# Kernel tuning notes

Hardware: AMD Instinct MI355X
Metric: run time of the kernel (lower is better)

The kernel has to match this reference:

```python
import jax, jax.numpy as jnp
import numpy as np

H, W = 16, 64
HK, WK = 7, 11
NUM_HEADS = 8
DIM = 512
HEAD_DIM = DIM // NUM_HEADS
SCALE = HEAD_DIM ** -0.5
N = H * W


def _local_mask():
    # Additive mask [N, N]: 0 inside the local window, -inf outside.
    # Equivalent to the torch loop: token (h,w) attends to (i,j) with
    # |i-h| <= HK//2 and |j-w| <= WK//2 (odd kernel, centered crop).
    h = jnp.arange(H)
    w = jnp.arange(W)
    hh, ww = jnp.meshgrid(h, w, indexing='ij')  # [H, W]
    q_h = hh.reshape(-1)  # [N]
    q_w = ww.reshape(-1)
    in_win = (jnp.abs(q_h[:, None] - q_h[None, :]) <= HK // 2) & \
             (jnp.abs(q_w[:, None] - q_w[None, :]) <= WK // 2)
    return jnp.where(in_win, 0.0, -jnp.inf).astype(jnp.float32)  # [N, N]


def setup_inputs() -> dict:
    key = jax.random.key(0)
    k1, k2, k3 = jax.random.split(key, 3)
    x = jax.random.normal(k1, (64, N, DIM), dtype=jnp.float32)
    w_qkv = jax.random.normal(k2, (DIM, 3 * DIM), dtype=jnp.float32) * 0.02
    w_proj = jax.random.normal(k3, (DIM, DIM), dtype=jnp.float32) * 0.02
    b_proj = jnp.zeros((DIM,), dtype=jnp.float32)
    return {"x": x, "w_qkv": w_qkv, "w_proj": w_proj, "b_proj": b_proj}


def reference(x, w_qkv, w_proj, b_proj):
    B = x.shape[0]
    mask = _local_mask()  # [N, N]
    qkv = (x @ w_qkv).reshape(B, N, 3, NUM_HEADS, HEAD_DIM)
    q = qkv[:, :, 0].transpose(0, 2, 1, 3) * SCALE  # [B, h, N, d]
    k = qkv[:, :, 1].transpose(0, 2, 1, 3)
    v = qkv[:, :, 2].transpose(0, 2, 1, 3)
    attn = jnp.einsum('bhnd,bhmd->bhnm', q, k) + mask  # [B, h, N, N]
    attn = jax.nn.softmax(attn, axis=-1)
    out = jnp.einsum('bhnm,bhmd->bhnd', attn, v)
    out = out.transpose(0, 2, 1, 3).reshape(B, N, DIM)
    return out @ w_proj + b_proj
```

## Files before the change

kernel.cpp:

```cpp
#include <hip/hip_runtime.h>
#include <hip/hip_bf16.h>
#include <stdint.h>

#define HGRID   16
#define WGRID   64
#define NTOK    1024
#define BATCH   64
#define NHEADS  8
#define HDIM    64
#define DMODEL  512
#define BH_TOT  512
#define QK_SCALE (0.125f * 1.44269504089f)

typedef __attribute__((ext_vector_type(8))) short short8;
typedef __attribute__((ext_vector_type(4))) float floatx4;

__device__ __forceinline__ short f2bf(float f) {
    union { float f; uint32_t u; } c{f};
    uint32_t r = (c.u + 0x7fffu + ((c.u >> 16) & 1u)) >> 16;
    return (short)r;
}

__device__ __forceinline__ void gload_lds16(const void* g, void* l) {
    auto gp = (const __attribute__((address_space(1))) void*)(uintptr_t)g;
    auto lp = (__attribute__((address_space(3))) void*)(uint32_t)(uintptr_t)l;
    __builtin_amdgcn_global_load_lds(gp, lp, 16, 0, 0);
}

__global__ __launch_bounds__(256)
void cast_x_kernel(const float* __restrict__ in, short* __restrict__ out) {
    size_t i = (size_t)blockIdx.x * 256 + threadIdx.x;
    const float4* in4 = (const float4*)in;
    float4 a = in4[i * 2];
    float4 b = in4[i * 2 + 1];
    short8 o;
    o[0] = f2bf(a.x); o[1] = f2bf(a.y); o[2] = f2bf(a.z); o[3] = f2bf(a.w);
    o[4] = f2bf(b.x); o[5] = f2bf(b.y); o[6] = f2bf(b.z); o[7] = f2bf(b.w);
    *(short8*)(out + i * 8) = o;
}

__global__ __launch_bounds__(256)
void tcast_kernel(const float* __restrict__ in, short* __restrict__ out, int R, int C) {
    __shared__ short tile[64][72];
    int r0 = blockIdx.x * 64, c0 = blockIdx.y * 64;
    int t = threadIdx.x;
#pragma unroll
    for (int i = 0; i < 16; i++) {
        int s = i * 256 + t;
        int r = s >> 6, c = s & 63;
        tile[r][c] = f2bf(in[(size_t)(r0 + r) * C + c0 + c]);
    }
    __syncthreads();
#pragma unroll
    for (int i = 0; i < 16; i++) {
        int s = i * 256 + t;
        int c = s >> 6, r = s & 63;
        out[(size_t)(c0 + c) * R + r0 + r] = tile[r][c];
    }
}

template <int MODE>
__global__ __launch_bounds__(256)
void gemm_kernel(const short* __restrict__ A, const short* __restrict__ Bm,
                 short* __restrict__ qo, short* __restrict__ ko, short* __restrict__ vo,
                 float* __restrict__ outf, const float* __restrict__ bias) {
    __shared__ short As[128 * 32];
    __shared__ short Bs[128 * 32];
    const int bn = blockIdx.x, bm = blockIdx.y;
    const int t = threadIdx.x;
    const int w = t >> 6;
    const int l = t & 63;
    const int wm = w >> 1, wn = w & 1;
    const int lq = l & 15, quad = l >> 4;

    const floatx4 zero = {0.f, 0.f, 0.f, 0.f};
    floatx4 acc[4][4];
#pragma unroll
    for (int i = 0; i < 4; i++)
#pragma unroll
        for (int j = 0; j < 4; j++) acc[i][j] = zero;

    const short* Ab = A + (size_t)bm * 128 * 512;
    const short* Bb = Bm + (size_t)bn * 128 * 512;

    for (int k0 = 0; k0 < 512; k0 += 32) {
        __syncthreads();
#pragma unroll
        for (int i = 0; i < 2; i++) {
            int s = i * 256 + t;
            int r = s >> 2, c8 = (s & 3) * 8;
            gload_lds16(Ab + (size_t)r * 512 + k0 + c8, &As[s * 8]);
            gload_lds16(Bb + (size_t)r * 512 + k0 + c8, &Bs[s * 8]);
        }
        __syncthreads();

        short8 af[4], bfr[4];
#pragma unroll
        for (int mi = 0; mi < 4; mi++)
            af[mi] = *(const short8*)&As[(wm * 64 + mi * 16 + lq) * 32 + quad * 8];
#pragma unroll
        for (int ni = 0; ni < 4; ni++)
            bfr[ni] = *(const short8*)&Bs[(wn * 64 + ni * 16 + lq) * 32 + quad * 8];
#pragma unroll
        for (int mi = 0; mi < 4; mi++)
#pragma unroll
            for (int ni = 0; ni < 4; ni++)
                acc[mi][ni] = __builtin_amdgcn_mfma_f32_16x16x32_bf16(
                    af[mi], bfr[ni], acc[mi][ni], 0, 0, 0);
    }

#pragma unroll
    for (int mi = 0; mi < 4; mi++)
#pragma unroll
        for (int ni = 0; ni < 4; ni++)
#pragma unroll
            for (int r = 0; r < 4; r++) {
                int row = bm * 128 + wm * 64 + mi * 16 + quad * 4 + r;
                int col = bn * 128 + wn * 64 + ni * 16 + lq;
                float val = acc[mi][ni][r];
                if (MODE == 0) {
                    int bidx = row >> 10, tok = row & 1023;
                    int which = col >> 9, hd = (col >> 6) & 7, dd = col & 63;
                    size_t didx = (((size_t)bidx * NHEADS + hd) * NTOK + tok) * HDIM + dd;
                    if (which == 0)       qo[didx] = f2bf(val * QK_SCALE);
                    else if (which == 1)  ko[didx] = f2bf(val);
                    else                  vo[didx] = f2bf(val);
                } else {
                    outf[(size_t)row * DMODEL + col] = val + bias[col];
                }
            }
}

__global__ __launch_bounds__(256)
void tv_kernel(const short* __restrict__ v, short* __restrict__ vT) {
    __shared__ short tile[64][72];
    int tt = blockIdx.x;
    int bh = blockIdx.y;
    int t = threadIdx.x;
    const short* src = v + ((size_t)bh * NTOK + tt * 64) * HDIM;
#pragma unroll
    for (int i = 0; i < 2; i++) {
        int s = i * 256 + t;
        int r = s >> 3, c8 = (s & 7) * 8;
        *(short8*)&tile[r][c8] = *(const short8*)(src + r * HDIM + c8);
    }
    __syncthreads();
    short* dst = vT + (size_t)bh * HDIM * NTOK + tt * 64;
#pragma unroll
    for (int i = 0; i < 2; i++) {
        int s = i * 256 + t;
        int d = s & 63, t0 = (s >> 6) * 8;
        short8 g;
#pragma unroll
        for (int j = 0; j < 8; j++) g[j] = tile[t0 + j][d];
        *(short8*)(dst + (size_t)d * NTOK + t0) = g;
    }
}

__global__ __launch_bounds__(256)
void attn_kernel(const short* __restrict__ q, const short* __restrict__ k,
                 const short* __restrict__ vT, short* __restrict__ ao) {
    const int bid = blockIdx.x;
    const int h = (bid >> 3) & 15;
    const int bh = (bid & 7) + 8 * (bid >> 7);
    const int b = bh >> 3, head = bh & 7;
    const int t = threadIdx.x;
    const int w = t >> 6;
    const int l = t & 63;
    const int lq = l & 15, quad = l >> 4;

    __shared__ short Kc[64][72];
    __shared__ short Vc[80][72];
    __shared__ short Pc[4][16][40];

    const int s_w = (w == 0) ? 0 : (w == 1) ? 8 : (w == 2) ? 24 : 32;

    const short* qbp = q + ((size_t)bh * NTOK + h * 64 + w * 16 + lq) * HDIM + quad * 8;
    short8 qa0 = *(const short8*)(qbp);
    short8 qa1 = *(const short8*)(qbp + 32);

    bool ok[2][4];
#pragma unroll
    for (int nt = 0; nt < 2; nt++)
#pragma unroll
        for (int r = 0; r < 4; r++) {
            int kw_g = s_w + nt * 16 + lq;
            int qi = w * 16 + quad * 4 + r;
            int dw = kw_g - qi;
            ok[nt][r] = (dw <= 5) && (dw >= -5);
        }

    const floatx4 zero = {0.f, 0.f, 0.f, 0.f};
    floatx4 O[5];
#pragma unroll
    for (int i = 0; i < 5; i++) O[i] = zero;

    if (t < 64) Vc[64][t] = (short)0x3F80;

    const int kh0 = (h - 3 < 0) ? 0 : h - 3;
    const int kh1 = (h + 3 > HGRID - 1) ? HGRID - 1 : h + 3;

    for (int kh = kh0; kh <= kh1; ++kh) {
        __syncthreads();
        {
            const short* kb = k + ((size_t)bh * NTOK + kh * 64) * HDIM;
            const short* vb = vT + (size_t)bh * HDIM * NTOK + kh * 64;
#pragma unroll
            for (int i = 0; i < 2; i++) {
                int s = i * 256 + t;
                int r = s >> 3, c8 = (s & 7) * 8;
                *(short8*)&Kc[r][c8] = *(const short8*)(kb + r * HDIM + c8);
                *(short8*)&Vc[r][c8] = *(const short8*)(vb + (size_t)r * NTOK + c8);
            }
        }
        __syncthreads();

        floatx4 S[2];
#pragma unroll
        for (int nt = 0; nt < 2; nt++) {
            S[nt] = zero;
            short8 b0 = *(const short8*)&Kc[s_w + nt * 16 + lq][quad * 8];
            short8 b1 = *(const short8*)&Kc[s_w + nt * 16 + lq][quad * 8 + 32];
            S[nt] = __builtin_amdgcn_mfma_f32_16x16x32_bf16(qa0, b0, S[nt], 0, 0, 0);
            S[nt] = __builtin_amdgcn_mfma_f32_16x16x32_bf16(qa1, b1, S[nt], 0, 0, 0);
        }

#pragma unroll
        for (int nt = 0; nt < 2; nt++)
#pragma unroll
            for (int r = 0; r < 4; r++) {
                float p = ok[nt][r] ? exp2f(S[nt][r]) : 0.f;
                Pc[w][quad * 4 + r][nt * 16 + lq] = f2bf(p);
            }

        short8 pa = *(const short8*)&Pc[w][lq][quad * 8];
#pragma unroll
        for (int dt = 0; dt < 5; dt++) {
            short8 vf = *(const short8*)&Vc[dt * 16 + lq][s_w + quad * 8];
            O[dt] = __builtin_amdgcn_mfma_f32_16x16x32_bf16(pa, vf, O[dt], 0, 0, 0);
        }
    }

    float inv[4];
#pragma unroll
    for (int r = 0; r < 4; r++) {
        float s = __shfl(O[4][r], l & 48);
        inv[r] = 1.0f / s;
    }

#pragma unroll
    for (int dt = 0; dt < 4; dt++)
#pragma unroll
        for (int r = 0; r < 4; r++) {
            int qi = w * 16 + quad * 4 + r;
            int d = dt * 16 + lq;
            float o = O[dt][r] * inv[r];
            ao[((size_t)b * NTOK + h * 64 + qi) * DMODEL + head * HDIM + d] = f2bf(o);
        }
}

extern "C" void kernel_launch(void* const* d_in, const int* in_sizes, int n_in,
                              void* d_out, int out_size, void* d_ws, size_t ws_size,
                              hipStream_t stream) {
    const float* x      = (const float*)d_in[0];
    const float* w_qkv  = (const float*)d_in[1];
    const float* w_proj = (const float*)d_in[2];
    const float* b_proj = (const float*)d_in[3];
    float* out = (float*)d_out;

    const size_t SZ_X    = (size_t)BATCH * NTOK * DMODEL * 2;
    const size_t SZ_HEAD = (size_t)BH_TOT * NTOK * HDIM * 2;
    char* p = (char*)d_ws;
    short* xb     = (short*)p; p += SZ_X;
    short* wqkvT  = (short*)p; p += (size_t)1536 * 512 * 2;
    short* wprojT = (short*)p; p += (size_t)512 * 512 * 2;
    short* qb     = (short*)p; p += SZ_HEAD;
    short* kb     = (short*)p; p += SZ_HEAD;
    short* vb     = (short*)p; p += SZ_HEAD;
    short* vTb    = (short*)p; p += SZ_HEAD;
    short* ao     = xb;

    cast_x_kernel<<<dim3((BATCH * NTOK * DMODEL) / (256 * 8)), dim3(256), 0, stream>>>(x, xb);
    tcast_kernel<<<dim3(512 / 64, 1536 / 64), dim3(256), 0, stream>>>(w_qkv, wqkvT, 512, 1536);
    tcast_kernel<<<dim3(512 / 64, 512 / 64), dim3(256), 0, stream>>>(w_proj, wprojT, 512, 512);
    gemm_kernel<0><<<dim3(1536 / 128, 65536 / 128), dim3(256), 0, stream>>>(
        xb, wqkvT, qb, kb, vb, nullptr, nullptr);
    tv_kernel<<<dim3(NTOK / 64, BH_TOT), dim3(256), 0, stream>>>(vb, vTb);
    attn_kernel<<<dim3(HGRID * BH_TOT), dim3(256), 0, stream>>>(qb, kb, vTb, ao);
    gemm_kernel<1><<<dim3(512 / 128, 65536 / 128), dim3(256), 0, stream>>>(
        ao, wprojT, nullptr, nullptr, nullptr, out, b_proj);
}
```

Measured before the change: 559.6 us.

## Replace GEMM with 256x256-tile, 8-wave, double-buffered swizzled LDS pipeline

Both projection GEMMs now use a new kernel with 512 threads and 256x256 output tiles. It keeps 128 KB of LDS in two buffers with an XOR swizzle, and issues direct global-to-LDS prefetches of the next K-slice interleaved with MFMA phases, using explicit barriers, waitcnt and setprio. It also remaps the block ID across groups of eight for better L2 locality. The aim is to raise MFMA utilisation and hide global load latency compared with the old single-buffered 128x128 kernel. In exchange it uses many registers and 128 KB of LDS per block, and its hand-tuned synchronisation is fragile.

```diff
diff --git a/kernel.cpp b/kernel.cpp
--- a/kernel.cpp
+++ b/kernel.cpp
@@ -25,6 +25,11 @@
     auto gp = (const __attribute__((address_space(1))) void*)(uintptr_t)g;
     auto lp = (__attribute__((address_space(3))) void*)(uint32_t)(uintptr_t)l;
     __builtin_amdgcn_global_load_lds(gp, lp, 16, 0, 0);
+}
+
+__device__ __forceinline__ void stage2(const short* g, char* l) {
+    gload_lds16(g, l);
+    gload_lds16(g + 32, l + 8192);
 }
 
 __global__ __launch_bounds__(256)
@@ -60,75 +65,198 @@
 }
 
 template <int MODE>
-__global__ __launch_bounds__(256)
-void gemm_kernel(const short* __restrict__ A, const short* __restrict__ Bm,
-                 short* __restrict__ qo, short* __restrict__ ko, short* __restrict__ vo,
-                 float* __restrict__ outf, const float* __restrict__ bias) {
-    __shared__ short As[128 * 32];
-    __shared__ short Bs[128 * 32];
-    const int bn = blockIdx.x, bm = blockIdx.y;
+__global__ __launch_bounds__(512, 2)
+void gemm8_kernel(const short* __restrict__ A, const short* __restrict__ Bm,
+                  short* __restrict__ qo, short* __restrict__ ko, short* __restrict__ vo,
+                  float* __restrict__ outf, const float* __restrict__ bias) {
+    constexpr int NBN = (MODE == 0) ? 6 : 2;
+    constexpr int NWG = (MODE == 0) ? 1536 : 512;
+    __shared__ short lds[65536];
+    char* ldsc = (char*)lds;
+
+    int bid = blockIdx.x;
+    bid = (bid & 7) * (NWG >> 3) + (bid >> 3);
+    const int bn = bid % NBN, bm = bid / NBN;
+
     const int t = threadIdx.x;
-    const int w = t >> 6;
-    const int l = t & 63;
-    const int wm = w >> 1, wn = w & 1;
+    const int w = t >> 6, l = t & 63;
     const int lq = l & 15, quad = l >> 4;
+    const int wm = w >> 2, wn = w & 3;
+
+    const int sw32 = ((lq >> 3) & 1) << 5;
+    const int qb16 = (quad * 16) ^ sw32;
+    const int a_lane = wm * 16384 + lq * 64 + qb16;
+    const int b_lane = 32768 + (wn >> 1) * 16384 + (wn & 1) * 4096 + lq * 64 + qb16;
+    const int t16 = t * 16;
+
+    const int srow = t >> 2;
+    const int scol = ((t & 3) * 8) ^ (((t >> 5) & 1) << 4);
+    const short* gA = A + (size_t)bm * 256 * 512 + (size_t)srow * 512 + scol;
+    const short* gB = Bm + (size_t)bn * 256 * 512 + (size_t)srow * 512 + scol;
 
     const floatx4 zero = {0.f, 0.f, 0.f, 0.f};
-    floatx4 acc[4][4];
-#pragma unroll
-    for (int i = 0; i < 4; i++)
+    floatx4 acc[8][4];
+#pragma unroll
+    for (int i = 0; i < 8; i++)
 #pragma unroll
         for (int j = 0; j < 4; j++) acc[i][j] = zero;
 
-    const short* Ab = A + (size_t)bm * 128 * 512;
-    const short* Bb = Bm + (size_t)bn * 128 * 512;
-
-    for (int k0 = 0; k0 < 512; k0 += 32) {
-        __syncthreads();
-#pragma unroll
-        for (int i = 0; i < 2; i++) {
-            int s = i * 256 + t;
-            int r = s >> 2, c8 = (s & 3) * 8;
-            gload_lds16(Ab + (size_t)r * 512 + k0 + c8, &As[s * 8]);
-            gload_lds16(Bb + (size_t)r * 512 + k0 + c8, &Bs[s * 8]);
-        }
-        __syncthreads();
-
-        short8 af[4], bfr[4];
-#pragma unroll
-        for (int mi = 0; mi < 4; mi++)
-            af[mi] = *(const short8*)&As[(wm * 64 + mi * 16 + lq) * 32 + quad * 8];
-#pragma unroll
-        for (int ni = 0; ni < 4; ni++)
-            bfr[ni] = *(const short8*)&Bs[(wn * 64 + ni * 16 + lq) * 32 + quad * 8];
-#pragma unroll
-        for (int mi = 0; mi < 4; mi++)
+    stage2(gA,              ldsc + t16);
+    stage2(gA + 65536,      ldsc + 16384 + t16);
+    stage2(gB,              ldsc + 32768 + t16);
+    stage2(gB + 65536,      ldsc + 49152 + t16);
+    stage2(gB + 64,         ldsc + 98304 + t16);
+    stage2(gB + 65536 + 64, ldsc + 114688 + t16);
+    asm volatile("s_waitcnt vmcnt(4)" ::: "memory");
+    __builtin_amdgcn_s_barrier();
+
+#pragma unroll 2
+    for (int T = 0; T < 8; ++T) {
+        const int bo  = (T & 1) << 16;
+        const int nbo = bo ^ 65536;
+        short8 bfr[4][2];
+
+        {
+            short8 af[2][2];
 #pragma unroll
             for (int ni = 0; ni < 4; ni++)
-                acc[mi][ni] = __builtin_amdgcn_mfma_f32_16x16x32_bf16(
-                    af[mi], bfr[ni], acc[mi][ni], 0, 0, 0);
-    }
-
-#pragma unroll
-    for (int mi = 0; mi < 4; mi++)
-#pragma unroll
-        for (int ni = 0; ni < 4; ni++)
-#pragma unroll
-            for (int r = 0; r < 4; r++) {
-                int row = bm * 128 + wm * 64 + mi * 16 + quad * 4 + r;
-                int col = bn * 128 + wn * 64 + ni * 16 + lq;
-                float val = acc[mi][ni][r];
-                if (MODE == 0) {
+#pragma unroll
+                for (int kh = 0; kh < 2; kh++)
+                    bfr[ni][kh] = *(const short8*)(ldsc + bo + b_lane + ni * 1024 + kh * 8192);
+#pragma unroll
+            for (int m2 = 0; m2 < 2; m2++)
+#pragma unroll
+                for (int kh = 0; kh < 2; kh++)
+                    af[m2][kh] = *(const short8*)(ldsc + bo + a_lane + m2 * 1024 + kh * 8192);
+            if (T < 7) stage2(gA + (T + 1) * 64, ldsc + nbo + t16);
+            __builtin_amdgcn_sched_barrier(0);
+            __builtin_amdgcn_s_barrier();
+            asm volatile("s_waitcnt lgkmcnt(0)" ::: "memory");
+            __builtin_amdgcn_sched_barrier(0);
+            __builtin_amdgcn_s_setprio(1);
+#pragma unroll
+            for (int kh = 0; kh < 2; kh++)
+#pragma unroll
+                for (int m2 = 0; m2 < 2; m2++)
+#pragma unroll
+                    for (int ni = 0; ni < 4; ni++)
+                        acc[m2][ni] = __builtin_amdgcn_mfma_f32_16x16x32_bf16(
+                            af[m2][kh], bfr[ni][kh], acc[m2][ni], 0, 0, 0);
+            __builtin_amdgcn_s_setprio(0);
+            __builtin_amdgcn_sched_barrier(0);
+            __builtin_amdgcn_s_barrier();
+        }
+        {
+            short8 af[2][2];
+#pragma unroll
+            for (int m2 = 0; m2 < 2; m2++)
+#pragma unroll
+                for (int kh = 0; kh < 2; kh++)
+                    af[m2][kh] = *(const short8*)(ldsc + bo + a_lane + (2 + m2) * 1024 + kh * 8192);
+            if (T < 7) stage2(gA + 65536 + (T + 1) * 64, ldsc + nbo + 16384 + t16);
+            __builtin_amdgcn_sched_barrier(0);
+            __builtin_amdgcn_s_barrier();
+            asm volatile("s_waitcnt lgkmcnt(0)" ::: "memory");
+            __builtin_amdgcn_sched_barrier(0);
+            __builtin_amdgcn_s_setprio(1);
+#pragma unroll
+            for (int kh = 0; kh < 2; kh++)
+#pragma unroll
+                for (int m2 = 0; m2 < 2; m2++)
+#pragma unroll
+                    for (int ni = 0; ni < 4; ni++)
+                        acc[2 + m2][ni] = __builtin_amdgcn_mfma_f32_16x16x32_bf16(
+                            af[m2][kh], bfr[ni][kh], acc[2 + m2][ni], 0, 0, 0);
+            __builtin_amdgcn_s_setprio(0);
+            __builtin_amdgcn_sched_barrier(0);
+            __builtin_amdgcn_s_barrier();
+        }
+        {
+            short8 af[2][2];
+#pragma unroll
+            for (int m2 = 0; m2 < 2; m2++)
+#pragma unroll
+                for (int kh = 0; kh < 2; kh++)
+                    af[m2][kh] = *(const short8*)(ldsc + bo + a_lane + (4 + m2) * 1024 + kh * 8192);
+            if (T < 6) stage2(gB + (T + 2) * 64, ldsc + bo + 32768 + t16);
+            __builtin_amdgcn_sched_barrier(0);
+            __builtin_amdgcn_s_barrier();
+            asm volatile("s_waitcnt lgkmcnt(0)" ::: "memory");
+            __builtin_amdgcn_sched_barrier(0);
+            __builtin_amdgcn_s_setprio(1);
+#pragma unroll
+            for (int kh = 0; kh < 2; kh++)
+#pragma unroll
+                for (int m2 = 0; m2 < 2; m2++)
+#pragma unroll
+                    for (int ni = 0; ni < 4; ni++)
+                        acc[4 + m2][ni] = __builtin_amdgcn_mfma_f32_16x16x32_bf16(
+                            af[m2][kh], bfr[ni][kh], acc[4 + m2][ni], 0, 0, 0);
+            __builtin_amdgcn_s_setprio(0);
+            __builtin_amdgcn_sched_barrier(0);
+            __builtin_amdgcn_s_barrier();
+        }
+        {
+            short8 af[2][2];
+#pragma unroll
+            for (int m2 = 0; m2 < 2; m2++)
+#pragma unroll
+                for (int kh = 0; kh < 2; kh++)
+                    af[m2][kh] = *(const short8*)(ldsc + bo + a_lane + (6 + m2) * 1024 + kh * 8192);
+            if (T < 6) stage2(gB + 65536 + (T + 2) * 64, ldsc + bo + 49152 + t16);
+            __builtin_amdgcn_sched_barrier(0);
+            __builtin_amdgcn_s_barrier();
+            asm volatile("s_waitcnt lgkmcnt(0)" ::: "memory");
+            __builtin_amdgcn_sched_barrier(0);
+            __builtin_amdgcn_s_setprio(1);
+#pragma unroll
+            for (int kh = 0; kh < 2; kh++)
+#pragma unroll
+                for (int m2 = 0; m2 < 2; m2++)
+#pragma unroll
+                    for (int ni = 0; ni < 4; ni++)
+                        acc[6 + m2][ni] = __builtin_amdgcn_mfma_f32_16x16x32_bf16(
+                            af[m2][kh], bfr[ni][kh], acc[6 + m2][ni], 0, 0, 0);
+            __builtin_amdgcn_s_setprio(0);
+            __builtin_amdgcn_sched_barrier(0);
+            if (T < 6) asm volatile("s_waitcnt vmcnt(4)" ::: "memory");
+            else       asm volatile("s_waitcnt vmcnt(0)" ::: "memory");
+            __builtin_amdgcn_s_barrier();
+        }
+    }
+
+    if (MODE == 0) {
+#pragma unroll
+        for (int mi = 0; mi < 8; mi++)
+#pragma unroll
+            for (int ni = 0; ni < 4; ni++) {
+                int col = bn * 256 + wn * 64 + ni * 16 + lq;
+                int which = col >> 9, hd = (col >> 6) & 7, dd = col & 63;
+#pragma unroll
+                for (int r = 0; r < 4; r++) {
+                    int row = bm * 256 + wm * 128 + mi * 16 + quad * 4 + r;
                     int bidx = row >> 10, tok = row & 1023;
-                    int which = col >> 9, hd = (col >> 6) & 7, dd = col & 63;
                     size_t didx = (((size_t)bidx * NHEADS + hd) * NTOK + tok) * HDIM + dd;
+                    float val = acc[mi][ni][r];
                     if (which == 0)       qo[didx] = f2bf(val * QK_SCALE);
                     else if (which == 1)  ko[didx] = f2bf(val);
                     else                  vo[didx] = f2bf(val);
-                } else {
-                    outf[(size_t)row * DMODEL + col] = val + bias[col];
                 }
             }
+    } else {
+#pragma unroll
+        for (int ni = 0; ni < 4; ni++) {
+            int col = bn * 256 + wn * 64 + ni * 16 + lq;
+            float bv = bias[col];
+#pragma unroll
+            for (int mi = 0; mi < 8; mi++)
+#pragma unroll
+                for (int r = 0; r < 4; r++) {
+                    int row = bm * 256 + wm * 128 + mi * 16 + quad * 4 + r;
+                    outf[(size_t)row * DMODEL + col] = acc[mi][ni][r] + bv;
+                }
+        }
+    }
 }
 
 __global__ __launch_bounds__(256)
@@ -283,10 +411,8 @@
     cast_x_kernel<<<dim3((BATCH * NTOK * DMODEL) / (256 * 8)), dim3(256), 0, stream>>>(x, xb);
     tcast_kernel<<<dim3(512 / 64, 1536 / 64), dim3(256), 0, stream>>>(w_qkv, wqkvT, 512, 1536);
     tcast_kernel<<<dim3(512 / 64, 512 / 64), dim3(256), 0, stream>>>(w_proj, wprojT, 512, 512);
-    gemm_kernel<0><<<dim3(1536 / 128, 65536 / 128), dim3(256), 0, stream>>>(
-        xb, wqkvT, qb, kb, vb, nullptr, nullptr);
+    gemm8_kernel<0><<<dim3(1536), dim3(512), 0, stream>>>(xb, wqkvT, qb, kb, vb, nullptr, nullptr);
     tv_kernel<<<dim3(NTOK / 64, BH_TOT), dim3(256), 0, stream>>>(vb, vTb);
     attn_kernel<<<dim3(HGRID * BH_TOT), dim3(256), 0, stream>>>(qb, kb, vTb, ao);
-    gemm_kernel<1><<<dim3(512 / 128, 65536 / 128), dim3(256), 0, stream>>>(
-        ao, wprojT, nullptr, nullptr, nullptr, out, b_proj);
-}
+    gemm8_kernel<1><<<dim3(512), dim3(512), 0, stream>>>(ao, wprojT, nullptr, nullptr, nullptr, out, b_proj);
+}
```

Result: faster. 536.0 us (-4.2%).
